# Optimization experiments

Measured on AMD Instinct MI355X. Metric: run time of the kernel, lower is better.

The kernel has to match this reference:

```python
import jax, jax.numpy as jnp
import numpy as np

T_STEPS = 4
LAYERS = 10
CYCLE = 10
C = 64
TAU = 1.2
V_TH = 0.5
SG_ALPHA = 4.0  # spikingjelly default surrogate.Sigmoid alpha


@jax.custom_vjp
def heaviside_sg(x):
    return (x >= 0.0).astype(x.dtype)

def _h_fwd(x):
    return heaviside_sg(x), x

def _h_bwd(x, g):
    s = jax.nn.sigmoid(SG_ALPHA * x)
    return (SG_ALPHA * s * (1.0 - s) * g,)

heaviside_sg.defvjp(_h_fwd, _h_bwd)


def lif(x_seq):
    # MultiStepLIFNode: v' = v + (x - (v - v_reset))/tau, hard reset to v_reset=0,
    # detach_reset=True -> spike in reset path is stop-gradient'ed.
    def step(v, x):
        v = v + (x - v) / TAU
        spike = heaviside_sg(v - V_TH)
        v = v * (1.0 - jax.lax.stop_gradient(spike))
        return v, spike
    _, spikes = jax.lax.scan(step, jnp.zeros_like(x_seq[0]), x_seq)
    return spikes


def conv_seq(x, w, b, dilation=1):
    # x: [T,B,Cin,L]; w: [Cout,Cin,K]; 'same' padding for odd K
    T, B, Ci, L = x.shape
    K = w.shape[-1]
    pad = (K - 1) * dilation // 2
    y = jax.lax.conv_general_dilated(
        x.reshape(T * B, Ci, L), w, (1,), [(pad, pad)],
        rhs_dilation=(dilation,), dimension_numbers=('NCH', 'OIH', 'NCH'))
    y = y + b[None, :, None]
    return y.reshape(T, B, -1, L)


def setup_inputs() -> dict:
    key = jax.random.key(0)
    ks = jax.random.split(key, 20)
    B, L = 4, 4096
    s = 0.1
    n = jax.random.normal
    inp = {
        'audio': jax.random.uniform(ks[0], (B, L), dtype=jnp.float32),
        'diffusion_step': jax.random.randint(ks[1], (B,), 0, 50),
        'W_in': n(ks[2], (C, 1, 1), jnp.float32) * s,
        'b_in': n(ks[3], (C,), jnp.float32) * s,
        'demb_w1': n(ks[4], (LAYERS, C, 1), jnp.float32) * s,
        'demb_b1': n(ks[5], (LAYERS, C), jnp.float32) * s,
        'demb_w2': n(ks[6], (LAYERS, C, C), jnp.float32) * s,
        'demb_b2': n(ks[7], (LAYERS, C), jnp.float32) * s,
        'dproj_w': n(ks[8], (LAYERS, C, C), jnp.float32) * s,
        'dproj_b': n(ks[9], (LAYERS, C), jnp.float32) * s,
        'conv_w': n(ks[10], (LAYERS, 2 * C, C, 3), jnp.float32) * 0.05,
        'conv_b': n(ks[11], (LAYERS, 2 * C), jnp.float32) * s,
        'skip_w': n(ks[12], (LAYERS, C, C, 1), jnp.float32) * s,
        'skip_b': n(ks[13], (LAYERS, C), jnp.float32) * s,
        'res_w': n(ks[14], (LAYERS, C, C, 1), jnp.float32) * s,
        'res_b': n(ks[15], (LAYERS, C), jnp.float32) * s,
        'W_out': n(ks[16], (1, C, 1), jnp.float32) * s,
        'b_out': n(ks[17], (1,), jnp.float32) * s,
    }
    return inp


def reference(audio, diffusion_step, W_in, b_in, demb_w1, demb_b1, demb_w2,
              demb_b2, dproj_w, dproj_b, conv_w, conv_b, skip_w, skip_b,
              res_w, res_b, W_out, b_out):
    B, L = audio.shape
    # Poisson encoder: spike = 1[u < x] per timestep (fixed key -> deterministic)
    u = jax.random.uniform(jax.random.key(42), (T_STEPS, B, 1, L), dtype=jnp.float32)
    spike_seq = (u < audio[None, :, None, :]).astype(jnp.float32)

    x = conv_seq(spike_seq, W_in, b_in)          # [T,B,C,L]
    x = lif(x)

    d = diffusion_step.astype(jnp.float32)[:, None]  # [B,1]
    total_skip = jnp.zeros_like(x)
    for i in range(LAYERS):
        dilation = 2 ** (i % CYCLE)
        emb = jax.nn.silu(d @ demb_w1[i].T + demb_b1[i]) @ demb_w2[i].T + demb_b2[i]  # [B,C]
        proj = emb @ dproj_w[i].T + dproj_b[i]                                        # [B,C]
        y = x + proj[None, :, :, None]
        y = conv_seq(y, conv_w[i], conv_b[i], dilation=dilation)  # [T,B,2C,L]
        y = lif(y)
        gate, filt = jnp.split(y, 2, axis=2)
        y = jax.nn.sigmoid(gate) * jnp.tanh(filt)
        total_skip = total_skip + conv_seq(y, skip_w[i], skip_b[i])
        x = x + conv_seq(y, res_w[i], res_b[i])

    total_skip = jax.nn.relu(total_skip)
    out = conv_seq(total_skip, W_out, b_out)  # [T,B,1,L]
    out = lif(out)
    return out.sum(axis=0)  # [B,1,L]
```

## Files before the change

### kernel.cpp

```cpp
#include <hip/hip_runtime.h>

#define LL 4096
#define NB 4
#define NC 64
#define NT 4
#define NLAYERS 10
#define XS 5120
#define XPAD 512

typedef float v2f __attribute__((ext_vector_type(2)));

typedef __attribute__((address_space(4))) const float cfloat;
__device__ __forceinline__ cfloat* to_constant(const float* p) {
  return (cfloat*)(unsigned long long)p;
}

__device__ __forceinline__ void threefry2x32(unsigned x0, unsigned x1,
                                             unsigned& o0, unsigned& o1) {
  const unsigned ks0 = 0u, ks1 = 42u;
  const unsigned ks2 = 0x1BD11BDAu ^ ks0 ^ ks1;
  const unsigned ks[3] = {ks0, ks1, ks2};
  const unsigned r0[4] = {13u, 15u, 26u, 6u};
  const unsigned r1[4] = {17u, 29u, 16u, 24u};
  x0 += ks0; x1 += ks1;
#pragma unroll
  for (int g = 0; g < 5; ++g) {
    const unsigned* rr = (g & 1) ? r1 : r0;
#pragma unroll
    for (int j = 0; j < 4; ++j) {
      x0 += x1;
      unsigned r = rr[j];
      x1 = (x1 << r) | (x1 >> (32u - r));
      x1 ^= x0;
    }
    x0 += ks[(g + 1) % 3];
    x1 += ks[(g + 2) % 3] + (unsigned)(g + 1);
  }
  o0 = x0; o1 = x1;
}

__device__ __forceinline__ float u01(unsigned bits) {
  return __uint_as_float((bits >> 9) | 0x3f800000u) - 1.0f;
}

__device__ __forceinline__ float lif_step(float& v, float xt) {
  v = v + (xt - v) / 1.2f;
  float s = (v >= 0.5f) ? 1.0f : 0.0f;
  v = v * (1.0f - s);
  return s;
}

__global__ void prep_kernel(const float* __restrict__ skip_w,
                            const float* __restrict__ res_w,
                            const float* __restrict__ conv_w,
                            float* __restrict__ skipT,
                            float* __restrict__ resT,
                            float* __restrict__ wT) {
  int i = blockIdx.x;
  for (int idx = threadIdx.x; idx < 4096; idx += 256) {
    int c = idx >> 6, cp = idx & 63;
    skipT[i * 4096 + cp * 64 + c] = skip_w[i * 4096 + c * 64 + cp];
    resT[i * 4096 + cp * 64 + c] = res_w[i * 4096 + c * 64 + cp];
  }
  for (int idx = threadIdx.x; idx < 16 * 64 * 3 * 8; idx += 256) {
    int col = idx & 7;
    int r = idx >> 3;
    int k = r % 3; r /= 3;
    int ci = r % 64;
    int g = r / 64;
    int co = (col < 4) ? (g * 4 + col) : (64 + g * 4 + (col - 4));
    wT[i * 24576 + idx] = conv_w[(i * 128 + co) * 192 + ci * 3 + k];
  }
}

__global__ void proj_kernel(const int* __restrict__ dstep,
                            const float* __restrict__ w1, const float* __restrict__ b1,
                            const float* __restrict__ w2, const float* __restrict__ b2,
                            const float* __restrict__ pw, const float* __restrict__ pb,
                            float* __restrict__ proj) {
  __shared__ float e1[NB][NC];
  __shared__ float e2[NB][NC];
  int i = blockIdx.x;
  int tid = threadIdx.x;
  int b = tid >> 6, c = tid & 63;
  float d = (float)dstep[b];
  float v = d * w1[i * 64 + c] + b1[i * 64 + c];
  v = v / (1.0f + expf(-v));
  e1[b][c] = v;
  __syncthreads();
  float a = b2[i * 64 + c];
  for (int cp = 0; cp < 64; ++cp) a += e1[b][cp] * w2[(i * 64 + c) * 64 + cp];
  e2[b][c] = a;
  __syncthreads();
  float p = pb[i * 64 + c];
  for (int cp = 0; cp < 64; ++cp) p += e2[b][cp] * pw[(i * 64 + c) * 64 + cp];
  proj[(i * 4 + b) * 64 + c] = p;
}

__global__ void pc_kernel(const float* __restrict__ proj,
                          const float* __restrict__ conv_w,
                          float* __restrict__ pc) {
  __shared__ float pv[64];
  int layer = blockIdx.x, b = blockIdx.y;
  int tid = threadIdx.x;
  if (tid < 64) pv[tid] = proj[(layer * 4 + b) * 64 + tid];
  __syncthreads();
  int co = tid;
  const float* w = conv_w + (layer * 128 + co) * 192;
  float s0 = 0.0f, s1 = 0.0f, s2 = 0.0f;
  for (int ci = 0; ci < 64; ++ci) {
    float p = pv[ci];
    s0 += p * w[ci * 3 + 0];
    s1 += p * w[ci * 3 + 1];
    s2 += p * w[ci * 3 + 2];
  }
  float* o = pc + ((layer * 4 + b) * 128 + co) * 3;
  o[0] = s0; o[1] = s1; o[2] = s2;
}

__global__ void padzero_kernel(float* __restrict__ x) {
  int row = blockIdx.x;
  float* base = x + (size_t)row * XS * 4;
  for (int i = threadIdx.x; i < XPAD; i += 256) {
    *(float4*)&base[i * 4] = float4{0.f, 0.f, 0.f, 0.f};
    *(float4*)&base[(XPAD + LL + i) * 4] = float4{0.f, 0.f, 0.f, 0.f};
  }
}

__global__ void encode_lif_kernel(const float* __restrict__ audio,
                                  const float* __restrict__ W_in,
                                  const float* __restrict__ b_in,
                                  float* __restrict__ x) {
  int tid = threadIdx.x;
  int lq = tid & 63, grp = tid >> 6;
  int l = blockIdx.x * 64 + lq;
  int b = blockIdx.y;
  float a = audio[b * LL + l];
  unsigned p0 = (unsigned)(b * LL + l);
  unsigned p1 = 16384u + p0;
  unsigned o00, o01, o10, o11;
  threefry2x32(p0, p0 + 32768u, o00, o01);
  threefry2x32(p1, p1 + 32768u, o10, o11);
  float sp[4];
  sp[0] = (u01(o00) < a) ? 1.0f : 0.0f;
  sp[1] = (u01(o10) < a) ? 1.0f : 0.0f;
  sp[2] = (u01(o01) < a) ? 1.0f : 0.0f;
  sp[3] = (u01(o11) < a) ? 1.0f : 0.0f;
  for (int j = 0; j < 16; ++j) {
    int c = grp * 16 + j;
    float w = W_in[c], bb = b_in[c];
    float v = 0.0f;
    float4 o;
    float* op = (float*)&o;
#pragma unroll
    for (int t = 0; t < 4; ++t) op[t] = lif_step(v, w * sp[t] + bb);
    *(float4*)&x[(size_t)((b * 64 + c) * XS + XPAD + l) * 4] = o;
  }
}

template <int DIL>
__global__ __launch_bounds__(256) void layer_conv_kernel(
    const float* __restrict__ x, const float* __restrict__ wT,
    const float* __restrict__ conv_b, const float* __restrict__ pc,
    float* __restrict__ y, int layer) {
  int tid = threadIdx.x;
  int g = blockIdx.y;
  int b = blockIdx.z;
  int l = blockIdx.x * 256 + tid;
  cfloat* cw = to_constant(wT + (size_t)(layer * 16 + g) * 1536);

  const float* px = x + (size_t)(b * 64 * XS + XPAD + l) * 4;

  float acc[8][4];
#pragma unroll
  for (int j = 0; j < 8; ++j)
#pragma unroll
    for (int t = 0; t < 4; ++t) acc[j][t] = 0.0f;

  float4 xa[3], xb[3];
  float wA[3][8], wB[3][8];

  auto loadx = [&](float4* dst) {
    dst[0] = *(const float4*)(px - (size_t)DIL * 4);
    dst[1] = *(const float4*)px;
    dst[2] = *(const float4*)(px + (size_t)DIL * 4);
    px += (size_t)XS * 4;
  };
  auto loadw = [&](int ci, float (*w)[8]) {
#pragma unroll
    for (int k = 0; k < 3; ++k)
#pragma unroll
      for (int j = 0; j < 8; ++j)
        w[k][j] = cw[(ci * 3 + k) * 8 + j];
  };
  auto compute = [&](const float (*w)[8], const float4* xv) {
#pragma unroll
    for (int k = 0; k < 3; ++k) {
      const float* xk = (const float*)&xv[k];
#pragma unroll
      for (int t = 0; t < 4; ++t) {
        float xq = xk[t];
#pragma unroll
        for (int j = 0; j < 8; ++j)
          acc[j][t] += w[k][j] * xq;
      }
    }
  };

  loadx(xa);
  loadw(0, wA);
  for (int ci = 0; ci < 64; ci += 2) {
    loadx(xb);
    loadw(ci + 1, wB);
    compute(wA, xa);
    if (ci + 2 < 64) {
      loadx(xa);
      loadw(ci + 2, wA);
    }
    compute(wB, xb);
  }

  const float SIG1 = 0.73105857863000489f;
  const float TANH1 = 0.76159415595576486f;
  bool lb = (l < DIL), rb = (l >= LL - DIL);
#pragma unroll
  for (int j = 0; j < 4; ++j) {
    int cog = g * 4 + j;
    int cof = 64 + g * 4 + j;
    const float* pg = pc + ((layer * 4 + b) * 128 + cog) * 3;
    const float* pf = pc + ((layer * 4 + b) * 128 + cof) * 3;
    float S0g = pg[0], S1g = pg[1], S2g = pg[2];
    float S0f = pf[0], S1f = pf[1], S2f = pf[2];
    float bg = conv_b[layer * 128 + cog] + S0g + S1g + S2g;
    float bf = conv_b[layer * 128 + cof] + S0f + S1f + S2f;
    bg -= (lb ? S0g : 0.0f) + (rb ? S2g : 0.0f);
    bf -= (lb ? S0f : 0.0f) + (rb ? S2f : 0.0f);
    float vg = 0.0f, vf = 0.0f;
    float4 o;
    float* op = (float*)&o;
#pragma unroll
    for (int t = 0; t < 4; ++t) {
      float av = acc[j][t];
      float fv = acc[j + 4][t];
      float sg = lif_step(vg, av + bg);
      float sf = lif_step(vf, fv + bf);
      float gv = (sg != 0.0f) ? SIG1 : 0.5f;
      float tv = (sf != 0.0f) ? TANH1 : 0.0f;
      op[t] = gv * tv;
    }
    *(float4*)&y[(size_t)((b * 64 + cog) * LL + l) * 4] = o;
  }
}

__global__ __launch_bounds__(256) void skip_res_kernel(
    const float* __restrict__ y, const float* __restrict__ skipT,
    const float* __restrict__ resT, const float* __restrict__ skip_b,
    const float* __restrict__ res_b, float* __restrict__ tskip,
    float* __restrict__ x, int layer) {
  int tid = threadIdx.x;
  int lg = tid & 15;
  int cg = tid >> 4;
  int b = blockIdx.y;
  int l0 = blockIdx.x * 32 + lg * 2;
  int c0 = cg * 4;

  const float* ws_ = skipT + layer * 4096 + c0;
  const float* wr_ = resT + layer * 4096 + c0;
  const float* yb = y + (size_t)(b * 64 * LL + l0) * 4;

  v2f as_[16], ar_[16];
#pragma unroll
  for (int q = 0; q < 16; ++q) {
    as_[q] = (v2f)(0.0f);
    ar_[q] = (v2f)(0.0f);
  }

  float4 wsa = *(const float4*)&ws_[0];
  float4 wra = *(const float4*)&wr_[0];
  float4 y0a = *(const float4*)yb;
  float4 y1a = *(const float4*)(yb + 4);

  for (int cp = 0; cp < 64; ++cp) {
    int cpn = (cp < 63) ? cp + 1 : 63;
    float4 wsb = *(const float4*)&ws_[cpn * 64];
    float4 wrb = *(const float4*)&wr_[cpn * 64];
    float4 y0b = *(const float4*)(yb + (size_t)cpn * LL * 4);
    float4 y1b = *(const float4*)(yb + (size_t)cpn * LL * 4 + 4);

    float wsv[4] = {wsa.x, wsa.y, wsa.z, wsa.w};
    float wrv[4] = {wra.x, wra.y, wra.z, wra.w};
    const v2f* yp0 = (const v2f*)&y0a;
    const v2f* yp1 = (const v2f*)&y1a;
#pragma unroll
    for (int i = 0; i < 4; ++i) {
      v2f w2s, w2r;
      w2s.x = wsv[i]; w2s.y = wsv[i];
      w2r.x = wrv[i]; w2r.y = wrv[i];
      as_[i * 4 + 0] += w2s * yp0[0];
      as_[i * 4 + 1] += w2s * yp0[1];
      as_[i * 4 + 2] += w2s * yp1[0];
      as_[i * 4 + 3] += w2s * yp1[1];
      ar_[i * 4 + 0] += w2r * yp0[0];
      ar_[i * 4 + 1] += w2r * yp0[1];
      ar_[i * 4 + 2] += w2r * yp1[0];
      ar_[i * 4 + 3] += w2r * yp1[1];
    }
    wsa = wsb; wra = wrb; y0a = y0b; y1a = y1b;
  }

#pragma unroll
  for (int i = 0; i < 4; ++i) {
    int c = c0 + i;
    float sb = skip_b[layer * 64 + c];
    float rb = res_b[layer * 64 + c];
    {
      size_t idx = (size_t)((b * 64 + c) * LL + l0) * 4;
      float4 o0, o1;
      if (layer == 0) {
        o0 = float4{0.f, 0.f, 0.f, 0.f};
        o1 = o0;
      } else {
        o0 = *(const float4*)&tskip[idx];
        o1 = *(const float4*)&tskip[idx + 4];
      }
      o0.x += as_[i * 4 + 0][0] + sb;
      o0.y += as_[i * 4 + 0][1] + sb;
      o0.z += as_[i * 4 + 1][0] + sb;
      o0.w += as_[i * 4 + 1][1] + sb;
      o1.x += as_[i * 4 + 2][0] + sb;
      o1.y += as_[i * 4 + 2][1] + sb;
      o1.z += as_[i * 4 + 3][0] + sb;
      o1.w += as_[i * 4 + 3][1] + sb;
      *(float4*)&tskip[idx] = o0;
      *(float4*)&tskip[idx + 4] = o1;
    }
    {
      size_t idx = (size_t)((b * 64 + c) * XS + XPAD + l0) * 4;
      float4 o0 = *(const float4*)&x[idx];
      float4 o1 = *(const float4*)&x[idx + 4];
      o0.x += ar_[i * 4 + 0][0] + rb;
      o0.y += ar_[i * 4 + 0][1] + rb;
      o0.z += ar_[i * 4 + 1][0] + rb;
      o0.w += ar_[i * 4 + 1][1] + rb;
      o1.x += ar_[i * 4 + 2][0] + rb;
      o1.y += ar_[i * 4 + 2][1] + rb;
      o1.z += ar_[i * 4 + 3][0] + rb;
      o1.w += ar_[i * 4 + 3][1] + rb;
      *(float4*)&x[idx] = o0;
      *(float4*)&x[idx + 4] = o1;
    }
  }
}

__global__ void out_kernel(const float* __restrict__ tskip,
                           const float* __restrict__ W_out,
                           const float* __restrict__ b_out,
                           float* __restrict__ out) {
  __shared__ float red[4][4][64];
  int tid = threadIdx.x;
  int lq = tid & 63, grp = tid >> 6;
  int l = blockIdx.x * 64 + lq;
  int b = blockIdx.y;
  float acc[4] = {0.0f, 0.0f, 0.0f, 0.0f};
  for (int j = 0; j < 16; ++j) {
    int c = grp * 16 + j;
    float w = W_out[c];
    float4 sv = *(const float4*)&tskip[(size_t)((b * 64 + c) * LL + l) * 4];
    acc[0] += fmaxf(sv.x, 0.0f) * w;
    acc[1] += fmaxf(sv.y, 0.0f) * w;
    acc[2] += fmaxf(sv.z, 0.0f) * w;
    acc[3] += fmaxf(sv.w, 0.0f) * w;
  }
#pragma unroll
  for (int t = 0; t < 4; ++t) red[grp][t][lq] = acc[t];
  __syncthreads();
  if (grp == 0) {
    float bo = b_out[0];
    float v = 0.0f, s = 0.0f;
#pragma unroll
    for (int t = 0; t < 4; ++t) {
      float a = red[0][t][lq] + red[1][t][lq] + red[2][t][lq] + red[3][t][lq] + bo;
      s += lif_step(v, a);
    }
    out[b * LL + l] = s;
  }
}

extern "C" void kernel_launch(void* const* d_in, const int* in_sizes, int n_in,
                              void* d_out, int out_size, void* d_ws, size_t ws_size,
                              hipStream_t stream) {
  const float* audio   = (const float*)d_in[0];
  const int*   dstep   = (const int*)d_in[1];
  const float* W_in    = (const float*)d_in[2];
  const float* b_in    = (const float*)d_in[3];
  const float* demb_w1 = (const float*)d_in[4];
  const float* demb_b1 = (const float*)d_in[5];
  const float* demb_w2 = (const float*)d_in[6];
  const float* demb_b2 = (const float*)d_in[7];
  const float* dproj_w = (const float*)d_in[8];
  const float* dproj_b = (const float*)d_in[9];
  const float* conv_w  = (const float*)d_in[10];
  const float* conv_b  = (const float*)d_in[11];
  const float* skip_w  = (const float*)d_in[12];
  const float* skip_b  = (const float*)d_in[13];
  const float* res_w   = (const float*)d_in[14];
  const float* res_b   = (const float*)d_in[15];
  const float* W_out   = (const float*)d_in[16];
  const float* b_out   = (const float*)d_in[17];
  float* out = (float*)d_out;
  float* ws = (float*)d_ws;

  float* proj  = ws;
  float* skipT = proj + 2560;
  float* resT  = skipT + 40960;
  float* pc    = resT + 40960;
  float* wT    = pc + 15360;
  float* x     = wT + 245760;
  float* y     = x + 5242880;
  float* tskip = y + 4194304;

  prep_kernel<<<10, 256, 0, stream>>>(skip_w, res_w, conv_w, skipT, resT, wT);
  proj_kernel<<<10, 256, 0, stream>>>(dstep, demb_w1, demb_b1, demb_w2, demb_b2,
                                      dproj_w, dproj_b, proj);
  pc_kernel<<<dim3(10, 4), 128, 0, stream>>>(proj, conv_w, pc);
  padzero_kernel<<<256, 256, 0, stream>>>(x);
  encode_lif_kernel<<<dim3(64, 4), 256, 0, stream>>>(audio, W_in, b_in, x);

  for (int i = 0; i < NLAYERS; ++i) {
    dim3 gc(16, 16, 4);
    switch (i) {
      case 0: layer_conv_kernel<1><<<gc, 256, 0, stream>>>(x, wT, conv_b, pc, y, i); break;
      case 1: layer_conv_kernel<2><<<gc, 256, 0, stream>>>(x, wT, conv_b, pc, y, i); break;
      case 2: layer_conv_kernel<4><<<gc, 256, 0, stream>>>(x, wT, conv_b, pc, y, i); break;
      case 3: layer_conv_kernel<8><<<gc, 256, 0, stream>>>(x, wT, conv_b, pc, y, i); break;
      case 4: layer_conv_kernel<16><<<gc, 256, 0, stream>>>(x, wT, conv_b, pc, y, i); break;
      case 5: layer_conv_kernel<32><<<gc, 256, 0, stream>>>(x, wT, conv_b, pc, y, i); break;
      case 6: layer_conv_kernel<64><<<gc, 256, 0, stream>>>(x, wT, conv_b, pc, y, i); break;
      case 7: layer_conv_kernel<128><<<gc, 256, 0, stream>>>(x, wT, conv_b, pc, y, i); break;
      case 8: layer_conv_kernel<256><<<gc, 256, 0, stream>>>(x, wT, conv_b, pc, y, i); break;
      case 9: layer_conv_kernel<512><<<gc, 256, 0, stream>>>(x, wT, conv_b, pc, y, i); break;
    }
    skip_res_kernel<<<dim3(128, 4), 256, 0, stream>>>(y, skipT, resT, skip_b,
                                                      res_b, tskip, x, i);
  }
  out_kernel<<<dim3(64, 4), 256, 0, stream>>>(tskip, W_out, b_out, out);
}
```

Baseline: 796.0 us.

## Deepen load prefetch in conv and skip/res loops; fuse setup kernels

The dilated conv kernel and the skip/res kernel now keep three channel loads in flight (four-slot rotating buffers) instead of one, so global-memory latency is hidden better inside the channel loop. The proj and pc kernels are merged into one kernel, and padding zeroing moves into the encode kernel, removing two launches. The deeper prefetch raises register pressure, which could lower occupancy.

```diff
diff --git a/kernel.cpp b/kernel.cpp
--- a/kernel.cpp
+++ b/kernel.cpp
@@ -73,13 +73,15 @@
   }
 }
 
-__global__ void proj_kernel(const int* __restrict__ dstep,
-                            const float* __restrict__ w1, const float* __restrict__ b1,
-                            const float* __restrict__ w2, const float* __restrict__ b2,
-                            const float* __restrict__ pw, const float* __restrict__ pb,
-                            float* __restrict__ proj) {
+__global__ void proj_pc_kernel(const int* __restrict__ dstep,
+                               const float* __restrict__ w1, const float* __restrict__ b1,
+                               const float* __restrict__ w2, const float* __restrict__ b2,
+                               const float* __restrict__ pw, const float* __restrict__ pb,
+                               const float* __restrict__ conv_w,
+                               float* __restrict__ pc) {
   __shared__ float e1[NB][NC];
   __shared__ float e2[NB][NC];
+  __shared__ float pv[NB][NC];
   int i = blockIdx.x;
   int tid = threadIdx.x;
   int b = tid >> 6, c = tid & 63;
@@ -94,36 +96,21 @@
   __syncthreads();
   float p = pb[i * 64 + c];
   for (int cp = 0; cp < 64; ++cp) p += e2[b][cp] * pw[(i * 64 + c) * 64 + cp];
-  proj[(i * 4 + b) * 64 + c] = p;
-}
-
-__global__ void pc_kernel(const float* __restrict__ proj,
-                          const float* __restrict__ conv_w,
-                          float* __restrict__ pc) {
-  __shared__ float pv[64];
-  int layer = blockIdx.x, b = blockIdx.y;
-  int tid = threadIdx.x;
-  if (tid < 64) pv[tid] = proj[(layer * 4 + b) * 64 + tid];
+  pv[b][c] = p;
   __syncthreads();
-  int co = tid;
-  const float* w = conv_w + (layer * 128 + co) * 192;
-  float s0 = 0.0f, s1 = 0.0f, s2 = 0.0f;
-  for (int ci = 0; ci < 64; ++ci) {
-    float p = pv[ci];
-    s0 += p * w[ci * 3 + 0];
-    s1 += p * w[ci * 3 + 1];
-    s2 += p * w[ci * 3 + 2];
-  }
-  float* o = pc + ((layer * 4 + b) * 128 + co) * 3;
-  o[0] = s0; o[1] = s1; o[2] = s2;
-}
-
-__global__ void padzero_kernel(float* __restrict__ x) {
-  int row = blockIdx.x;
-  float* base = x + (size_t)row * XS * 4;
-  for (int i = threadIdx.x; i < XPAD; i += 256) {
-    *(float4*)&base[i * 4] = float4{0.f, 0.f, 0.f, 0.f};
-    *(float4*)&base[(XPAD + LL + i) * 4] = float4{0.f, 0.f, 0.f, 0.f};
+  for (int oidx = tid; oidx < 512; oidx += 256) {
+    int bb = oidx >> 7;
+    int co = oidx & 127;
+    const float* w = conv_w + (i * 128 + co) * 192;
+    float s0 = 0.0f, s1 = 0.0f, s2 = 0.0f;
+    for (int ci = 0; ci < 64; ++ci) {
+      float pp = pv[bb][ci];
+      s0 += pp * w[ci * 3 + 0];
+      s1 += pp * w[ci * 3 + 1];
+      s2 += pp * w[ci * 3 + 2];
+    }
+    float* o = pc + ((i * 4 + bb) * 128 + co) * 3;
+    o[0] = s0; o[1] = s1; o[2] = s2;
   }
 }
 
@@ -135,6 +122,13 @@
   int lq = tid & 63, grp = tid >> 6;
   int l = blockIdx.x * 64 + lq;
   int b = blockIdx.y;
+  {
+    float* base = x + (size_t)((b * 64 + blockIdx.x) * XS) * 4;
+    for (int q = tid; q < XPAD; q += 256) {
+      *(float4*)&base[q * 4] = float4{0.f, 0.f, 0.f, 0.f};
+      *(float4*)&base[(XPAD + LL + q) * 4] = float4{0.f, 0.f, 0.f, 0.f};
+    }
+  }
   float a = audio[b * LL + l];
   unsigned p0 = (unsigned)(b * LL + l);
   unsigned p1 = 16384u + p0;
@@ -177,7 +171,7 @@
 #pragma unroll
     for (int t = 0; t < 4; ++t) acc[j][t] = 0.0f;
 
-  float4 xa[3], xb[3];
+  float4 X[4][3];
   float wA[3][8], wB[3][8];
 
   auto loadx = [&](float4* dst) {
@@ -207,17 +201,23 @@
     }
   };
 
-  loadx(xa);
+  loadx(X[0]);
+  loadx(X[1]);
+  loadx(X[2]);
   loadw(0, wA);
-  for (int ci = 0; ci < 64; ci += 2) {
-    loadx(xb);
+  for (int ci = 0; ci < 64; ci += 4) {
     loadw(ci + 1, wB);
-    compute(wA, xa);
-    if (ci + 2 < 64) {
-      loadx(xa);
-      loadw(ci + 2, wA);
-    }
-    compute(wB, xb);
+    loadx(X[3]);
+    compute(wA, X[0]);
+    loadw(ci + 2, wA);
+    if (ci + 4 < 64) loadx(X[0]);
+    compute(wB, X[1]);
+    loadw(ci + 3, wB);
+    if (ci + 5 < 64) loadx(X[1]);
+    compute(wA, X[2]);
+    loadw((ci + 4 < 64) ? (ci + 4) : 0, wA);
+    if (ci + 6 < 64) loadx(X[2]);
+    compute(wB, X[3]);
   }
 
   const float SIG1 = 0.73105857863000489f;
@@ -275,22 +275,23 @@
     ar_[q] = (v2f)(0.0f);
   }
 
-  float4 wsa = *(const float4*)&ws_[0];
-  float4 wra = *(const float4*)&wr_[0];
-  float4 y0a = *(const float4*)yb;
-  float4 y1a = *(const float4*)(yb + 4);
-
-  for (int cp = 0; cp < 64; ++cp) {
-    int cpn = (cp < 63) ? cp + 1 : 63;
-    float4 wsb = *(const float4*)&ws_[cpn * 64];
-    float4 wrb = *(const float4*)&wr_[cpn * 64];
-    float4 y0b = *(const float4*)(yb + (size_t)cpn * LL * 4);
-    float4 y1b = *(const float4*)(yb + (size_t)cpn * LL * 4 + 4);
-
-    float wsv[4] = {wsa.x, wsa.y, wsa.z, wsa.w};
-    float wrv[4] = {wra.x, wra.y, wra.z, wra.w};
-    const v2f* yp0 = (const v2f*)&y0a;
-    const v2f* yp1 = (const v2f*)&y1a;
+  float4 Y0[4], Y1[4];
+  float4 wsa, wra, wsb, wrb;
+
+  auto loady = [&](float4& d0, float4& d1, int cp) {
+    d0 = *(const float4*)(yb + (size_t)cp * LL * 4);
+    d1 = *(const float4*)(yb + (size_t)cp * LL * 4 + 4);
+  };
+  auto loadwv = [&](float4& s, float4& r, int cp) {
+    s = *(const float4*)&ws_[cp * 64];
+    r = *(const float4*)&wr_[cp * 64];
+  };
+  auto compq = [&](const float4& wsv4, const float4& wrv4,
+                   const float4& yv0, const float4& yv1) {
+    float wsv[4] = {wsv4.x, wsv4.y, wsv4.z, wsv4.w};
+    float wrv[4] = {wrv4.x, wrv4.y, wrv4.z, wrv4.w};
+    const v2f* yp0 = (const v2f*)&yv0;
+    const v2f* yp1 = (const v2f*)&yv1;
 #pragma unroll
     for (int i = 0; i < 4; ++i) {
       v2f w2s, w2r;
@@ -305,7 +306,25 @@
       ar_[i * 4 + 2] += w2r * yp1[0];
       ar_[i * 4 + 3] += w2r * yp1[1];
     }
-    wsa = wsb; wra = wrb; y0a = y0b; y1a = y1b;
+  };
+
+  loady(Y0[0], Y1[0], 0);
+  loady(Y0[1], Y1[1], 1);
+  loady(Y0[2], Y1[2], 2);
+  loadwv(wsa, wra, 0);
+  for (int cp = 0; cp < 64; cp += 4) {
+    loadwv(wsb, wrb, cp + 1);
+    loady(Y0[3], Y1[3], cp + 3);
+    compq(wsa, wra, Y0[0], Y1[0]);
+    loadwv(wsa, wra, cp + 2);
+    if (cp + 4 < 64) loady(Y0[0], Y1[0], cp + 4);
+    compq(wsb, wrb, Y0[1], Y1[1]);
+    loadwv(wsb, wrb, cp + 3);
+    if (cp + 5 < 64) loady(Y0[1], Y1[1], cp + 5);
+    compq(wsa, wra, Y0[2], Y1[2]);
+    loadwv(wsa, wra, (cp + 4 < 64) ? (cp + 4) : 0);
+    if (cp + 6 < 64) loady(Y0[2], Y1[2], cp + 6);
+    compq(wsb, wrb, Y0[3], Y1[3]);
   }
 
 #pragma unroll
@@ -420,10 +439,8 @@
   float* tskip = y + 4194304;
 
   prep_kernel<<<10, 256, 0, stream>>>(skip_w, res_w, conv_w, skipT, resT, wT);
-  proj_kernel<<<10, 256, 0, stream>>>(dstep, demb_w1, demb_b1, demb_w2, demb_b2,
-                                      dproj_w, dproj_b, proj);
-  pc_kernel<<<dim3(10, 4), 128, 0, stream>>>(proj, conv_w, pc);
-  padzero_kernel<<<256, 256, 0, stream>>>(x);
+  proj_pc_kernel<<<10, 256, 0, stream>>>(dstep, demb_w1, demb_b1, demb_w2,
+                                         demb_b2, dproj_w, dproj_b, conv_w, pc);
   encode_lif_kernel<<<dim3(64, 4), 256, 0, stream>>>(audio, W_in, b_in, x);
 
   for (int i = 0; i < NLAYERS; ++i) {
```

Measured after the change: 860.8 us. +8.1%, slower.
